# Performance work log

Hardware: AMD Instinct MI355X
Metric: run time of the kernel (lower is better)

The kernel has to match this reference:

```python
import jax, jax.numpy as jnp
import numpy as np
from jax import lax


def _conv(x, w, b):
    # NCHW conv, 3x3, stride 1, SAME padding (matches nn.Conv2d(k=3, padding=1))
    y = lax.conv_general_dilated(x, w, (1, 1), 'SAME',
                                 dimension_numbers=('NCHW', 'OIHW', 'NCHW'))
    return y + b[None, :, None, None]


def _maxpool2(x):
    return lax.reduce_window(x, -jnp.inf, lax.max, (1, 1, 2, 2), (1, 1, 2, 2), 'VALID')


def setup_inputs() -> dict:
    key = jax.random.key(0)
    ks = jax.random.split(key, 8)
    B, C, H, W = 512, 3, 32, 32
    E, NC = 4, 100
    x = jax.random.normal(ks[0], (B, C, H, W), jnp.float32)
    s = lambda k, shape, fan: jax.random.normal(k, shape, jnp.float32) * (1.0 / np.sqrt(fan))
    return {
        'x': x,
        'r_conv_w': s(ks[1], (16, 3, 3, 3), 27),
        'r_conv_b': jnp.zeros((16,), jnp.float32),
        'r_fc_w': s(ks[2], (E, 16), 16),
        'r_fc_b': jnp.zeros((E,), jnp.float32),
        'e_w1': s(ks[3], (E, 32, 3, 3, 3), 27),
        'e_b1': jnp.zeros((E, 32), jnp.float32),
        'e_w2': s(ks[4], (E, 64, 32, 3, 3), 32 * 9),
        'e_b2': jnp.zeros((E, 64), jnp.float32),
        'e_fc_w': s(ks[5], (E, NC, 64 * 8 * 8), 64 * 8 * 8),
        'e_fc_b': jnp.zeros((E, NC), jnp.float32),
        'top_k': 1,
    }


def reference(x, r_conv_w, r_conv_b, r_fc_w, r_fc_b,
              e_w1, e_b1, e_w2, e_b2, e_fc_w, e_fc_b, top_k):
    E = r_fc_w.shape[0]
    # ---- router: conv -> relu -> global avg pool -> linear -> softmax ----
    h = jax.nn.relu(_conv(x, r_conv_w, r_conv_b))
    g = h.mean(axis=(2, 3))                                   # [B, 16]
    router_probs = jax.nn.softmax(g @ r_fc_w.T + r_fc_b, -1)   # [B, E]
    topk_prob, topk_idx = lax.top_k(router_probs, top_k)       # [B, K]

    # ---- experts (dense compute + weighted combine == hard dispatch/combine) ----
    def expert(w1, b1, w2, b2, fw, fb):
        h1 = _maxpool2(jax.nn.relu(_conv(x, w1, b1)))          # [B, 32, 16, 16]
        h2 = _maxpool2(jax.nn.relu(_conv(h1, w2, b2)))         # [B, 64, 8, 8]
        f = h2.reshape(h2.shape[0], -1)                        # [B, 4096]
        return f @ fw.T + fb                                   # [B, NC]

    expert_out = jax.vmap(expert)(e_w1, e_b1, e_w2, e_b2, e_fc_w, e_fc_b)  # [E, B, NC]

    onehot = jax.nn.one_hot(topk_idx, E, dtype=x.dtype)        # [B, K, E]
    comb_w = jnp.einsum('bke,bk->be', onehot, topk_prob)       # [B, E]
    final_output = jnp.einsum('ebc,be->bc', expert_out, comb_w)

    mean_probs = router_probs.mean(axis=0)
    aux_loss = jnp.mean((mean_probs - 1.0 / E) ** 2)
    return final_output, router_probs, aux_loss
```

## Files before the change

kernel.cpp:

```cpp
#include <hip/hip_runtime.h>
#include <hip/hip_bf16.h>
#include <math.h>

#define BATCH 512
#define NC 100

typedef __attribute__((ext_vector_type(8))) short bf16x8;
typedef __attribute__((ext_vector_type(4))) float f32x4;

__device__ inline ushort f2bf(float f) {
    __hip_bfloat16 h = __float2bfloat16(f);
    return *reinterpret_cast<ushort*>(&h);
}

__global__ __launch_bounds__(256) void cvt_all_kernel(const float* __restrict__ fw,
                                                      ushort* __restrict__ fwb,
                                                      const float* __restrict__ w2,
                                                      ushort* __restrict__ w2t,
                                                      const float* __restrict__ w1,
                                                      ushort* __restrict__ w1t)
{
    const int blk = blockIdx.x;
    if (blk < 1600) {
        const int i = (blk * 256 + threadIdx.x) * 4;
        float4 v = *(const float4*)(fw + i);
        ushort o[4];
        o[0] = f2bf(v.x); o[1] = f2bf(v.y); o[2] = f2bf(v.z); o[3] = f2bf(v.w);
        *(uint2*)(fwb + i) = *(uint2*)o;
    } else if (blk < 1888) {
        const int i = (blk - 1600) * 256 + threadIdx.x;
        const int ic = i & 31;
        const int oc = (i >> 5) & 63;
        const int et = i >> 11;
        const int e = et / 9, t = et % 9;
        w2t[i] = f2bf(w2[((e * 64 + oc) * 32 + ic) * 9 + t]);
    } else {
        const int i = (blk - 1888) * 256 + threadIdx.x;
        const int row = i >> 5, k = i & 31;
        w1t[i] = (k < 27) ? f2bf(w1[row * 27 + k]) : (ushort)0;
    }
}

__global__ __launch_bounds__(256) void fused_expert_kernel(
    const float* __restrict__ x,
    const float* __restrict__ rcw,
    const float* __restrict__ rcb,
    const float* __restrict__ rfw,
    const float* __restrict__ rfb,
    const ushort* __restrict__ w1t,
    const float* __restrict__ eb1,
    const ushort* __restrict__ w2t,
    const float* __restrict__ eb2,
    float* __restrict__ probs_out,
    int* __restrict__ sel,
    float* __restrict__ pw,
    uint* __restrict__ h2b)
{
    __shared__ float xs[3 * 34 * 40];
    __shared__ float rcb_s[16];
    __shared__ float rfw_s[68];
    __shared__ float red[4][16];
    __shared__ float g_s[16];
    __shared__ int   sel_s;
    __shared__ float eb1_s[128];
    __shared__ __align__(16) ushort A_s[18 * 18 * 32];

    const int b = blockIdx.x, tid = threadIdx.x;

    uint* A32 = (uint*)A_s;
    for (int i = tid; i < 1088; i += 256) {
        int y, xx, w;
        if (i < 576) { y = (i >= 288) ? 17 : 0; int r2 = i % 288; xx = r2 >> 4; w = r2 & 15; }
        else { int j = i - 576; y = 1 + (j >> 5); xx = ((j >> 4) & 1) ? 17 : 0; w = j & 15; }
        A32[(y * 18 + xx) * 16 + w] = 0u;
    }
    for (int i = tid; i < 3 * 34 * 40; i += 256) xs[i] = 0.f;
    if (tid < 128) eb1_s[tid] = eb1[tid];
    if (tid < 68) rfw_s[tid] = (tid < 64) ? rfw[tid] : rfb[tid - 64];
    if (tid >= 128 && tid < 144) rcb_s[tid - 128] = rcb[tid - 128];
    __syncthreads();
    const float* xb = x + b * 3072;
    for (int i = tid; i < 3072; i += 256) {
        int c = i >> 10, r = (i >> 5) & 31, cc = i & 31;
        xs[(c * 34 + r + 1) * 40 + (cc + 1)] = xb[i];
    }
    __syncthreads();

    {
        const int oc = tid & 15, pg = tid >> 4;
        float w[27];
#pragma unroll
        for (int j = 0; j < 27; ++j) w[j] = rcw[oc * 27 + j];
        const float bias = rcb_s[oc];
        float accm = 0.f;
#pragma unroll 1
        for (int ch = 0; ch < 2; ++ch) {
            const int c0 = ch * 16;
            float a0[16], a1[16];
#pragma unroll
            for (int j = 0; j < 16; ++j) { a0[j] = 0.f; a1[j] = 0.f; }
#pragma unroll
            for (int c = 0; c < 3; ++c) {
#pragma unroll
                for (int ry = 0; ry < 4; ++ry) {
                    const float* row = &xs[(c * 34 + 2 * pg + ry) * 40 + c0];
                    float rv[18];
                    float4 q0 = *(const float4*)(row);
                    float4 q1 = *(const float4*)(row + 4);
                    float4 q2 = *(const float4*)(row + 8);
                    float4 q3 = *(const float4*)(row + 12);
                    float2 q4 = *(const float2*)(row + 16);
                    rv[0] = q0.x; rv[1] = q0.y; rv[2] = q0.z; rv[3] = q0.w;
                    rv[4] = q1.x; rv[5] = q1.y; rv[6] = q1.z; rv[7] = q1.w;
                    rv[8] = q2.x; rv[9] = q2.y; rv[10] = q2.z; rv[11] = q2.w;
                    rv[12] = q3.x; rv[13] = q3.y; rv[14] = q3.z; rv[15] = q3.w;
                    rv[16] = q4.x; rv[17] = q4.y;
                    if (ry < 3) {
#pragma unroll
                        for (int kx = 0; kx < 3; ++kx) {
                            const float wv = w[c * 9 + ry * 3 + kx];
#pragma unroll
                            for (int j = 0; j < 16; ++j) a0[j] += wv * rv[j + kx];
                        }
                    }
                    if (ry > 0) {
#pragma unroll
                        for (int kx = 0; kx < 3; ++kx) {
                            const float wv = w[c * 9 + (ry - 1) * 3 + kx];
#pragma unroll
                            for (int j = 0; j < 16; ++j) a1[j] += wv * rv[j + kx];
                        }
                    }
                }
            }
#pragma unroll
            for (int j = 0; j < 16; ++j)
                accm += fmaxf(a0[j] + bias, 0.f) + fmaxf(a1[j] + bias, 0.f);
        }
        accm += __shfl_down(accm, 32);
        accm += __shfl_down(accm, 16);
        if ((tid & 63) < 16) red[tid >> 6][oc] = accm;
    }
    __syncthreads();
    if (tid < 16) g_s[tid] = (red[0][tid] + red[1][tid] + red[2][tid] + red[3][tid]) * (1.f / 1024.f);
    __syncthreads();

    if (tid == 0) {
        float logits[4];
#pragma unroll
        for (int e = 0; e < 4; ++e) {
            float s = rfw_s[64 + e];
#pragma unroll
            for (int o = 0; o < 16; ++o) s += g_s[o] * rfw_s[e * 16 + o];
            logits[e] = s;
        }
        float m = fmaxf(fmaxf(logits[0], logits[1]), fmaxf(logits[2], logits[3]));
        float ex[4], ssum = 0.f;
#pragma unroll
        for (int e = 0; e < 4; ++e) { ex[e] = __expf(logits[e] - m); ssum += ex[e]; }
        const float inv = 1.f / ssum;
        float p[4];
#pragma unroll
        for (int e = 0; e < 4; ++e) p[e] = ex[e] * inv;
        int am = 0; float best = p[0];
#pragma unroll
        for (int e = 1; e < 4; ++e) { if (p[e] > best) { best = p[e]; am = e; } }
        *(float4*)(probs_out + b * 4) = make_float4(p[0], p[1], p[2], p[3]);
        sel[b] = am;
        pw[b] = best;
        sel_s = am;
    }
    __syncthreads();
    const int e = sel_s;

    {
        const int wv = tid >> 6, lane = tid & 63;
        const int lr = lane & 15, kb = lane >> 4;
        const ushort* bsrc = w1t + (e * 32 + lr) * 32 + kb * 8;
        const bf16x8 b0 = *(const bf16x8*)(bsrc);
        const bf16x8 b1 = *(const bf16x8*)(bsrc + 16 * 32);
        const float bv0 = eb1_s[e * 32 + lr];
        const float bv1 = eb1_s[e * 32 + 16 + lr];

        int offj[8], valj[8];
#pragma unroll
        for (int jj = 0; jj < 8; ++jj) {
            int k = kb * 8 + jj;
            int ic = (k * 57) >> 9; ic = ic > 2 ? 2 : ic;
            int tap = k - ic * 9; tap = tap > 8 ? 8 : tap;
            int ky = (tap * 11) >> 5;
            int kx = tap - ky * 3;
            offj[jj] = (ic * 34 + ky) * 40 + kx;
            valj[jj] = (k < 27);
        }

#pragma unroll 2
        for (int mf = 0; mf < 16; ++mf) {
            const int pA = wv * 64 + mf * 4 + (lr >> 2);
            const int c2 = lr & 3;
            const int yA = ((pA >> 4) << 1) + (c2 >> 1);
            const int xA = ((pA & 15) << 1) + (c2 & 1);
            const int base = yA * 40 + xA;
            union { uint u[4]; bf16x8 v; } U;
#pragma unroll
            for (int jp = 0; jp < 4; ++jp) {
                float v0 = valj[2 * jp]     ? xs[base + offj[2 * jp]]     : 0.f;
                float v1 = valj[2 * jp + 1] ? xs[base + offj[2 * jp + 1]] : 0.f;
                U.u[jp] = (uint)f2bf(v0) | ((uint)f2bf(v1) << 16);
            }
            const f32x4 z = {0.f, 0.f, 0.f, 0.f};
            f32x4 c0 = __builtin_amdgcn_mfma_f32_16x16x32_bf16(U.v, b0, z, 0, 0, 0);
            f32x4 c1 = __builtin_amdgcn_mfma_f32_16x16x32_bf16(U.v, b1, z, 0, 0, 0);
            const int pp = wv * 64 + mf * 4 + kb;
            const int py = pp >> 4, px = pp & 15;
            ushort* dst = A_s + ((py + 1) * 18 + (px + 1)) * 32 + lr;
            float m0 = fmaxf(fmaxf(c0[0], c0[1]), fmaxf(c0[2], c0[3]));
            float m1 = fmaxf(fmaxf(c1[0], c1[1]), fmaxf(c1[2], c1[3]));
            dst[0]  = f2bf(fmaxf(m0 + bv0, 0.f));
            dst[16] = f2bf(fmaxf(m1 + bv1, 0.f));
        }
    }
    __syncthreads();

    const int wv = tid >> 6, lane = tid & 63;
    const int lr = lane & 15, kb = lane >> 4;
    const ushort* wgl = w2t + (size_t)e * 18432 + lr * 32 + kb * 8;

    f32x4 acc[4][4];
#pragma unroll
    for (int m = 0; m < 4; ++m)
#pragma unroll
        for (int n = 0; n < 4; ++n)
            acc[m][n] = (f32x4){0.f, 0.f, 0.f, 0.f};

#pragma unroll
    for (int t = 0; t < 9; ++t) {
        const int ky = t / 3, kx = t % 3;
        bf16x8 af[4], bfr[4];
#pragma unroll
        for (int m = 0; m < 4; ++m) {
            const int y = wv * 4 + m;
            af[m] = *(const bf16x8*)(A_s + ((y + ky) * 18 + (lr + kx)) * 32 + kb * 8);
        }
#pragma unroll
        for (int n = 0; n < 4; ++n)
            bfr[n] = *(const bf16x8*)(wgl + (t * 64 + n * 16) * 32);
#pragma unroll
        for (int m = 0; m < 4; ++m)
#pragma unroll
            for (int n = 0; n < 4; ++n)
                acc[m][n] = __builtin_amdgcn_mfma_f32_16x16x32_bf16(af[m], bfr[n], acc[m][n], 0, 0, 0);
    }

#pragma unroll
    for (int q = 0; q < 2; ++q) {
        const int py = wv * 2 + q;
#pragma unroll
        for (int n = 0; n < 4; ++n) {
            const int oc = n * 16 + lr;
            const float bn = eb2[e * 64 + oc];
            const f32x4 ca = acc[2 * q][n];
            const f32x4 cb = acc[2 * q + 1][n];
            float p0 = fmaxf(fmaxf(ca[0], ca[1]), fmaxf(cb[0], cb[1]));
            float p1 = fmaxf(fmaxf(ca[2], ca[3]), fmaxf(cb[2], cb[3]));
            float r0 = fmaxf(p0 + bn, 0.f);
            float r1 = fmaxf(p1 + bn, 0.f);
            uint pk = (uint)f2bf(r0) | ((uint)f2bf(r1) << 16);
            h2b[(size_t)b * 2048 + oc * 32 + py * 4 + kb] = pk;
        }
    }
}

__global__ __launch_bounds__(512) void scan_aux_kernel(const int* __restrict__ sel,
                                                       const float* __restrict__ probs,
                                                       int* __restrict__ ids,
                                                       int* __restrict__ offs,
                                                       float* __restrict__ aux_out)
{
    __shared__ int wcnt[4][8];
    __shared__ int wbase[4][8];
    __shared__ float wred[8][4];
    const int tid = threadIdx.x;
    const int wv = tid >> 6, lane = tid & 63;
    const int e = sel[tid];
    unsigned long long m[4];
#pragma unroll
    for (int k = 0; k < 4; ++k) m[k] = __ballot(e == k);
    if (lane == 0) {
#pragma unroll
        for (int k = 0; k < 4; ++k) wcnt[k][wv] = __popcll(m[k]);
    }
    float4 p = *(const float4*)(probs + tid * 4);
    float s0 = p.x, s1 = p.y, s2 = p.z, s3 = p.w;
#pragma unroll
    for (int off = 32; off > 0; off >>= 1) {
        s0 += __shfl_down(s0, off);
        s1 += __shfl_down(s1, off);
        s2 += __shfl_down(s2, off);
        s3 += __shfl_down(s3, off);
    }
    if (lane == 0) { wred[wv][0] = s0; wred[wv][1] = s1; wred[wv][2] = s2; wred[wv][3] = s3; }
    __syncthreads();
    if (tid == 0) {
        int o = 0;
        for (int k = 0; k < 4; ++k) {
            offs[k] = o;
            for (int w = 0; w < 8; ++w) { wbase[k][w] = o; o += wcnt[k][w]; }
        }
        offs[4] = o;
        float aux = 0.f;
#pragma unroll
        for (int k = 0; k < 4; ++k) {
            float t = 0.f;
            for (int w = 0; w < 8; ++w) t += wred[w][k];
            float mp = t * (1.f / BATCH) - 0.25f;
            aux += mp * mp;
        }
        aux_out[0] = aux * 0.25f;
    }
    __syncthreads();
    const unsigned long long below = (lane == 0) ? 0ull : (~0ull >> (64 - lane));
    const int rank = __popcll(m[e] & below);
    ids[wbase[e][wv] + rank] = tid;
}

__global__ __launch_bounds__(448) void fc_mfma_kernel(
    const ushort* __restrict__ h2b,
    const ushort* __restrict__ fwb,
    const int* __restrict__ ids,
    const int* __restrict__ offs,
    float* __restrict__ part)
{
    const int mt = blockIdx.x, ks = blockIdx.y, e = blockIdx.z;
    const int off = offs[e], cnt = offs[e + 1] - off;
    if (mt * 16 >= cnt) return;

    const int tid = threadIdx.x;
    const int wv = tid >> 6, lane = tid & 63;
    const int lr = lane & 15, kb = lane >> 4;
    const int cls = wv * 16 + lr;
    const int clsc = cls < NC ? cls : NC - 1;
    const int slot = mt * 16 + lr;
    const int sidx = ids[off + (slot < cnt ? slot : cnt - 1)];

    const ushort* ap = h2b + (size_t)sidx * 4096 + ks * 512 + kb * 8;
    const ushort* bp = fwb + (size_t)(e * NC + clsc) * 4096 + ks * 512 + kb * 8;

    f32x4 acc = {0.f, 0.f, 0.f, 0.f};
#pragma unroll
    for (int k = 0; k < 16; ++k) {
        bf16x8 a = *(const bf16x8*)(ap + k * 32);
        bf16x8 b = *(const bf16x8*)(bp + k * 32);
        acc = __builtin_amdgcn_mfma_f32_16x16x32_bf16(a, b, acc, 0, 0, 0);
    }

    if (cls < NC) {
#pragma unroll
        for (int j = 0; j < 4; ++j) {
            const int m = mt * 16 + kb * 4 + j;
            if (m < cnt) {
                const int sid = ids[off + m];
                part[((size_t)ks * 512 + sid) * NC + cls] = acc[j];
            }
        }
    }
}

__global__ __launch_bounds__(256) void fc_reduce_kernel(
    const float* __restrict__ part,
    const float* __restrict__ fb,
    const int* __restrict__ sel,
    const float* __restrict__ pw,
    float* __restrict__ outp)
{
    const int i = blockIdx.x * 256 + threadIdx.x;
    if (i >= BATCH * NC) return;
    const int s = i / NC, c = i - s * NC;
    float acc = 0.f;
#pragma unroll
    for (int k = 0; k < 8; ++k) acc += part[((size_t)k * 512 + s) * NC + c];
    outp[i] = pw[s] * (acc + fb[sel[s] * NC + c]);
}

extern "C" void kernel_launch(void* const* d_in, const int* in_sizes, int n_in,
                              void* d_out, int out_size, void* d_ws, size_t ws_size,
                              hipStream_t stream) {
    const float* x   = (const float*)d_in[0];
    const float* rcw = (const float*)d_in[1];
    const float* rcb = (const float*)d_in[2];
    const float* rfw = (const float*)d_in[3];
    const float* rfb = (const float*)d_in[4];
    const float* ew1 = (const float*)d_in[5];
    const float* eb1 = (const float*)d_in[6];
    const float* ew2 = (const float*)d_in[7];
    const float* eb2 = (const float*)d_in[8];
    const float* efw = (const float*)d_in[9];
    const float* efb = (const float*)d_in[10];
    (void)in_sizes; (void)n_in; (void)out_size; (void)ws_size;

    float* out       = (float*)d_out;
    float* final_out = out;
    float* probs_out = out + 51200;
    float* aux_out   = out + 53248;

    char* ws = (char*)d_ws;
    int*    sel  = (int*)ws;
    float*  pw   = (float*)(ws + 2048);
    int*    ids  = (int*)(ws + 4096);
    int*    offs = (int*)(ws + 6144);
    uint*   h2b  = (uint*)(ws + 8192);
    ushort* fwb  = (ushort*)(ws + 8192 + 4194304);
    ushort* w2t  = (ushort*)(ws + 8192 + 4194304 + 3276800);
    ushort* w1t  = (ushort*)(ws + 8192 + 4194304 + 3276800 + 147456);
    float*  part = (float*)(ws + 8192 + 4194304 + 3276800 + 147456 + 8192);

    cvt_all_kernel<<<1904, 256, 0, stream>>>(efw, fwb, ew2, w2t, ew1, w1t);
    fused_expert_kernel<<<512, 256, 0, stream>>>(x, rcw, rcb, rfw, rfb, w1t, eb1,
                                                 w2t, eb2, probs_out, sel, pw, h2b);
    scan_aux_kernel<<<1, 512, 0, stream>>>(sel, probs_out, ids, offs, aux_out);
    fc_mfma_kernel<<<dim3(32, 8, 4), 448, 0, stream>>>((const ushort*)h2b, fwb, ids, offs, part);
    fc_reduce_kernel<<<200, 256, 0, stream>>>(part, efb, sel, pw, final_out);
}
```

Baseline: 50.10 us.

## Double fused expert kernel threads to 512 and split work across 8 waves

Raises the fused expert kernel from 256 to 512 threads per block and repartitions each stage across the eight waves. The router conv halves are now handled by separate thread groups, conv1 MFMA tiles are split over 8 waves, and conv2 is split by output-channel halves. The aim is more latency hiding and shorter per-thread serial work per sample, since only 512 blocks exist. The cost is that each wave in conv2 reloads the A fragments, and the larger block may limit occupancy through registers or LDS.

```diff
diff --git a/kernel.cpp b/kernel.cpp
--- a/kernel.cpp
+++ b/kernel.cpp
@@ -41,7 +41,7 @@
     }
 }
 
-__global__ __launch_bounds__(256) void fused_expert_kernel(
+__global__ __launch_bounds__(512) void fused_expert_kernel(
     const float* __restrict__ x,
     const float* __restrict__ rcw,
     const float* __restrict__ rcb,
@@ -59,90 +59,95 @@
     __shared__ float xs[3 * 34 * 40];
     __shared__ float rcb_s[16];
     __shared__ float rfw_s[68];
-    __shared__ float red[4][16];
+    __shared__ float red[8][16];
     __shared__ float g_s[16];
     __shared__ int   sel_s;
     __shared__ float eb1_s[128];
     __shared__ __align__(16) ushort A_s[18 * 18 * 32];
 
     const int b = blockIdx.x, tid = threadIdx.x;
+    const int wvv = tid >> 6, lane = tid & 63;
+    const int lr = lane & 15, kb = lane >> 4;
 
     uint* A32 = (uint*)A_s;
-    for (int i = tid; i < 1088; i += 256) {
+    for (int i = tid; i < 1088; i += 512) {
         int y, xx, w;
         if (i < 576) { y = (i >= 288) ? 17 : 0; int r2 = i % 288; xx = r2 >> 4; w = r2 & 15; }
         else { int j = i - 576; y = 1 + (j >> 5); xx = ((j >> 4) & 1) ? 17 : 0; w = j & 15; }
         A32[(y * 18 + xx) * 16 + w] = 0u;
     }
-    for (int i = tid; i < 3 * 34 * 40; i += 256) xs[i] = 0.f;
+    for (int i = tid; i < 3 * 34 * 40; i += 512) xs[i] = 0.f;
     if (tid < 128) eb1_s[tid] = eb1[tid];
     if (tid < 68) rfw_s[tid] = (tid < 64) ? rfw[tid] : rfb[tid - 64];
     if (tid >= 128 && tid < 144) rcb_s[tid - 128] = rcb[tid - 128];
     __syncthreads();
     const float* xb = x + b * 3072;
-    for (int i = tid; i < 3072; i += 256) {
+    for (int i = tid; i < 3072; i += 512) {
         int c = i >> 10, r = (i >> 5) & 31, cc = i & 31;
         xs[(c * 34 + r + 1) * 40 + (cc + 1)] = xb[i];
     }
     __syncthreads();
 
     {
-        const int oc = tid & 15, pg = tid >> 4;
+        const int oc = tid & 15, sg = tid >> 4;
+        const int pg = sg & 15, half = sg >> 4;
+        const int c0 = half * 16;
         float w[27];
 #pragma unroll
         for (int j = 0; j < 27; ++j) w[j] = rcw[oc * 27 + j];
         const float bias = rcb_s[oc];
-        float accm = 0.f;
-#pragma unroll 1
-        for (int ch = 0; ch < 2; ++ch) {
-            const int c0 = ch * 16;
-            float a0[16], a1[16];
-#pragma unroll
-            for (int j = 0; j < 16; ++j) { a0[j] = 0.f; a1[j] = 0.f; }
-#pragma unroll
-            for (int c = 0; c < 3; ++c) {
-#pragma unroll
-                for (int ry = 0; ry < 4; ++ry) {
-                    const float* row = &xs[(c * 34 + 2 * pg + ry) * 40 + c0];
-                    float rv[18];
-                    float4 q0 = *(const float4*)(row);
-                    float4 q1 = *(const float4*)(row + 4);
-                    float4 q2 = *(const float4*)(row + 8);
-                    float4 q3 = *(const float4*)(row + 12);
-                    float2 q4 = *(const float2*)(row + 16);
-                    rv[0] = q0.x; rv[1] = q0.y; rv[2] = q0.z; rv[3] = q0.w;
-                    rv[4] = q1.x; rv[5] = q1.y; rv[6] = q1.z; rv[7] = q1.w;
-                    rv[8] = q2.x; rv[9] = q2.y; rv[10] = q2.z; rv[11] = q2.w;
-                    rv[12] = q3.x; rv[13] = q3.y; rv[14] = q3.z; rv[15] = q3.w;
-                    rv[16] = q4.x; rv[17] = q4.y;
-                    if (ry < 3) {
-#pragma unroll
-                        for (int kx = 0; kx < 3; ++kx) {
-                            const float wv = w[c * 9 + ry * 3 + kx];
-#pragma unroll
-                            for (int j = 0; j < 16; ++j) a0[j] += wv * rv[j + kx];
-                        }
+        float a0[16], a1[16];
+#pragma unroll
+        for (int j = 0; j < 16; ++j) { a0[j] = 0.f; a1[j] = 0.f; }
+#pragma unroll
+        for (int c = 0; c < 3; ++c) {
+#pragma unroll
+            for (int ry = 0; ry < 4; ++ry) {
+                const float* row = &xs[(c * 34 + 2 * pg + ry) * 40 + c0];
+                float rv[18];
+                float4 q0 = *(const float4*)(row);
+                float4 q1 = *(const float4*)(row + 4);
+                float4 q2 = *(const float4*)(row + 8);
+                float4 q3 = *(const float4*)(row + 12);
+                float2 q4 = *(const float2*)(row + 16);
+                rv[0] = q0.x; rv[1] = q0.y; rv[2] = q0.z; rv[3] = q0.w;
+                rv[4] = q1.x; rv[5] = q1.y; rv[6] = q1.z; rv[7] = q1.w;
+                rv[8] = q2.x; rv[9] = q2.y; rv[10] = q2.z; rv[11] = q2.w;
+                rv[12] = q3.x; rv[13] = q3.y; rv[14] = q3.z; rv[15] = q3.w;
+                rv[16] = q4.x; rv[17] = q4.y;
+                if (ry < 3) {
+#pragma unroll
+                    for (int kx = 0; kx < 3; ++kx) {
+                        const float wv = w[c * 9 + ry * 3 + kx];
+#pragma unroll
+                        for (int j = 0; j < 16; ++j) a0[j] += wv * rv[j + kx];
                     }
-                    if (ry > 0) {
-#pragma unroll
-                        for (int kx = 0; kx < 3; ++kx) {
-                            const float wv = w[c * 9 + (ry - 1) * 3 + kx];
-#pragma unroll
-                            for (int j = 0; j < 16; ++j) a1[j] += wv * rv[j + kx];
-                        }
+                }
+                if (ry > 0) {
+#pragma unroll
+                    for (int kx = 0; kx < 3; ++kx) {
+                        const float wv = w[c * 9 + (ry - 1) * 3 + kx];
+#pragma unroll
+                        for (int j = 0; j < 16; ++j) a1[j] += wv * rv[j + kx];
                     }
                 }
             }
-#pragma unroll
-            for (int j = 0; j < 16; ++j)
-                accm += fmaxf(a0[j] + bias, 0.f) + fmaxf(a1[j] + bias, 0.f);
-        }
+        }
+        float accm = 0.f;
+#pragma unroll
+        for (int j = 0; j < 16; ++j)
+            accm += fmaxf(a0[j] + bias, 0.f) + fmaxf(a1[j] + bias, 0.f);
         accm += __shfl_down(accm, 32);
         accm += __shfl_down(accm, 16);
-        if ((tid & 63) < 16) red[tid >> 6][oc] = accm;
-    }
-    __syncthreads();
-    if (tid < 16) g_s[tid] = (red[0][tid] + red[1][tid] + red[2][tid] + red[3][tid]) * (1.f / 1024.f);
+        if (lane < 16) red[wvv][lane] = accm;
+    }
+    __syncthreads();
+    if (tid < 16) {
+        float s = 0.f;
+#pragma unroll
+        for (int w = 0; w < 8; ++w) s += red[w][tid];
+        g_s[tid] = s * (1.f / 1024.f);
+    }
     __syncthreads();
 
     if (tid == 0) {
@@ -174,8 +179,6 @@
     const int e = sel_s;
 
     {
-        const int wv = tid >> 6, lane = tid & 63;
-        const int lr = lane & 15, kb = lane >> 4;
         const ushort* bsrc = w1t + (e * 32 + lr) * 32 + kb * 8;
         const bf16x8 b0 = *(const bf16x8*)(bsrc);
         const bf16x8 b1 = *(const bf16x8*)(bsrc + 16 * 32);
@@ -195,8 +198,8 @@
         }
 
 #pragma unroll 2
-        for (int mf = 0; mf < 16; ++mf) {
-            const int pA = wv * 64 + mf * 4 + (lr >> 2);
+        for (int mf = 0; mf < 8; ++mf) {
+            const int pA = wvv * 32 + mf * 4 + (lr >> 2);
             const int c2 = lr & 3;
             const int yA = ((pA >> 4) << 1) + (c2 >> 1);
             const int xA = ((pA & 15) << 1) + (c2 & 1);
@@ -211,7 +214,7 @@
             const f32x4 z = {0.f, 0.f, 0.f, 0.f};
             f32x4 c0 = __builtin_amdgcn_mfma_f32_16x16x32_bf16(U.v, b0, z, 0, 0, 0);
             f32x4 c1 = __builtin_amdgcn_mfma_f32_16x16x32_bf16(U.v, b1, z, 0, 0, 0);
-            const int pp = wv * 64 + mf * 4 + kb;
+            const int pp = wvv * 32 + mf * 4 + kb;
             const int py = pp >> 4, px = pp & 15;
             ushort* dst = A_s + ((py + 1) * 18 + (px + 1)) * 32 + lr;
             float m0 = fmaxf(fmaxf(c0[0], c0[1]), fmaxf(c0[2], c0[3]));
@@ -222,51 +225,52 @@
     }
     __syncthreads();
 
-    const int wv = tid >> 6, lane = tid & 63;
-    const int lr = lane & 15, kb = lane >> 4;
-    const ushort* wgl = w2t + (size_t)e * 18432 + lr * 32 + kb * 8;
-
-    f32x4 acc[4][4];
-#pragma unroll
-    for (int m = 0; m < 4; ++m)
-#pragma unroll
-        for (int n = 0; n < 4; ++n)
-            acc[m][n] = (f32x4){0.f, 0.f, 0.f, 0.f};
-
-#pragma unroll
-    for (int t = 0; t < 9; ++t) {
-        const int ky = t / 3, kx = t % 3;
-        bf16x8 af[4], bfr[4];
-#pragma unroll
-        for (int m = 0; m < 4; ++m) {
-            const int y = wv * 4 + m;
-            af[m] = *(const bf16x8*)(A_s + ((y + ky) * 18 + (lr + kx)) * 32 + kb * 8);
-        }
-#pragma unroll
-        for (int n = 0; n < 4; ++n)
-            bfr[n] = *(const bf16x8*)(wgl + (t * 64 + n * 16) * 32);
+    {
+        const int wy = wvv & 3, wn = wvv >> 2;
+        const ushort* wgl = w2t + (size_t)e * 18432 + lr * 32 + kb * 8;
+
+        f32x4 acc[4][2];
 #pragma unroll
         for (int m = 0; m < 4; ++m)
 #pragma unroll
-            for (int n = 0; n < 4; ++n)
-                acc[m][n] = __builtin_amdgcn_mfma_f32_16x16x32_bf16(af[m], bfr[n], acc[m][n], 0, 0, 0);
-    }
-
-#pragma unroll
-    for (int q = 0; q < 2; ++q) {
-        const int py = wv * 2 + q;
-#pragma unroll
-        for (int n = 0; n < 4; ++n) {
-            const int oc = n * 16 + lr;
-            const float bn = eb2[e * 64 + oc];
-            const f32x4 ca = acc[2 * q][n];
-            const f32x4 cb = acc[2 * q + 1][n];
-            float p0 = fmaxf(fmaxf(ca[0], ca[1]), fmaxf(cb[0], cb[1]));
-            float p1 = fmaxf(fmaxf(ca[2], ca[3]), fmaxf(cb[2], cb[3]));
-            float r0 = fmaxf(p0 + bn, 0.f);
-            float r1 = fmaxf(p1 + bn, 0.f);
-            uint pk = (uint)f2bf(r0) | ((uint)f2bf(r1) << 16);
-            h2b[(size_t)b * 2048 + oc * 32 + py * 4 + kb] = pk;
+            for (int n = 0; n < 2; ++n)
+                acc[m][n] = (f32x4){0.f, 0.f, 0.f, 0.f};
+
+#pragma unroll
+        for (int t = 0; t < 9; ++t) {
+            const int ky = t / 3, kx = t % 3;
+            bf16x8 af[4], bfr[2];
+#pragma unroll
+            for (int m = 0; m < 4; ++m) {
+                const int y = wy * 4 + m;
+                af[m] = *(const bf16x8*)(A_s + ((y + ky) * 18 + (lr + kx)) * 32 + kb * 8);
+            }
+#pragma unroll
+            for (int n = 0; n < 2; ++n)
+                bfr[n] = *(const bf16x8*)(wgl + (t * 64 + (wn * 2 + n) * 16) * 32);
+#pragma unroll
+            for (int m = 0; m < 4; ++m)
+#pragma unroll
+                for (int n = 0; n < 2; ++n)
+                    acc[m][n] = __builtin_amdgcn_mfma_f32_16x16x32_bf16(af[m], bfr[n], acc[m][n], 0, 0, 0);
+        }
+
+#pragma unroll
+        for (int q = 0; q < 2; ++q) {
+            const int py = wy * 2 + q;
+#pragma unroll
+            for (int n = 0; n < 2; ++n) {
+                const int oc = (wn * 2 + n) * 16 + lr;
+                const float bn = eb2[e * 64 + oc];
+                const f32x4 ca = acc[2 * q][n];
+                const f32x4 cb = acc[2 * q + 1][n];
+                float p0 = fmaxf(fmaxf(ca[0], ca[1]), fmaxf(cb[0], cb[1]));
+                float p1 = fmaxf(fmaxf(ca[2], ca[3]), fmaxf(cb[2], cb[3]));
+                float r0 = fmaxf(p0 + bn, 0.f);
+                float r1 = fmaxf(p1 + bn, 0.f);
+                uint pk = (uint)f2bf(r0) | ((uint)f2bf(r1) << 16);
+                h2b[(size_t)b * 2048 + oc * 32 + py * 4 + kb] = pk;
+            }
         }
     }
 }
@@ -415,7 +419,7 @@
     float*  part = (float*)(ws + 8192 + 4194304 + 3276800 + 147456 + 8192);
 
     cvt_all_kernel<<<1904, 256, 0, stream>>>(efw, fwb, ew2, w2t, ew1, w1t);
-    fused_expert_kernel<<<512, 256, 0, stream>>>(x, rcw, rcb, rfw, rfb, w1t, eb1,
+    fused_expert_kernel<<<512, 512, 0, stream>>>(x, rcw, rcb, rfw, rfb, w1t, eb1,
                                                  w2t, eb2, probs_out, sel, pw, h2b);
     scan_aux_kernel<<<1, 512, 0, stream>>>(sel, probs_out, ids, offs, aux_out);
     fc_mfma_kernel<<<dim3(32, 8, 4), 448, 0, stream>>>((const ushort*)h2b, fwb, ids, offs, part);
```

Measured after the change: 42.86 us. 14.5% less time.
